# Optimization experiments

Hardware: AMD Instinct MI355X
Metric: run time of the kernel (lower is better)

Reference implementation:

```python
import jax, jax.numpy as jnp
import numpy as np

# ---- module hyperparameters (from init_kwargs) ----
B, C, T = 4, 512, 400
K = 31            # kernel_size
STRIDE = 1
WP = 3            # weight_precision -> WP-1 = 2 paired memristor arrays
# DacAdcHardwareSettings
IN_BITS = 8
OUT_PREC = 8
OUT_RANGE = 10
VMAX = 0.6
CUR_SCALE = 8020.0
DAC_SCALE = 1.0 / 2 ** (IN_BITS - 1)
DAC_MIN, DAC_MAX = -(2 ** (IN_BITS - 1)), 2 ** (IN_BITS - 1)
ADC_SCALE = 1.0 / 2 ** OUT_PREC
ADC_MIN, ADC_MAX = -(2 ** (OUT_PREC + OUT_RANGE - 1)), 2 ** (OUT_PREC + OUT_RANGE - 1)
# memristor noise model constants
KBT = 1.380649e-23 * 300.0
BW = 1e-8
E = float(np.exp(1.0))
EPS = 1e-12
INPUT_FACTOR = 1.0
OUTPUT_FACTOR = 1.0


def fake_quant(x, scale, qmin, qmax):
    # torch.fake_quantize_per_tensor_affine with zero_point=0, STE gradient inside range
    q = jnp.round(x / scale)
    qc = jnp.clip(q, qmin, qmax) * scale
    mask = (q >= qmin) & (q <= qmax)
    return jnp.where(mask, x + jax.lax.stop_gradient(qc - x), jax.lax.stop_gradient(qc))


def polyval_asc(coeffs, x):
    # coefficients in ascending degree order (as in poly_mul); Horner over static length
    res = jnp.zeros_like(x)
    for c in coeffs[::-1]:
        res = res * x + c
    return res


def setup_inputs() -> dict:
    key = jax.random.key(0)
    k1, k2, k3, k4, k5 = jax.random.split(key, 5)
    x = jax.random.normal(k1, (B, C, T), dtype=jnp.float32)
    poly_low = jax.random.normal(k2, (WP - 1, 2, 7), dtype=jnp.float32)   # [bit, pos/neg, low_degree]
    poly_high = jax.random.normal(k3, (WP - 1, 2, 6), dtype=jnp.float32)  # [bit, pos/neg, high_degree]
    r = jax.random.uniform(k4, (WP - 1, 2, C, K), dtype=jnp.float32)      # blend factor per cell
    bias = jax.random.normal(k5, (C,), dtype=jnp.float32)
    return {"x": x, "poly_low": poly_low, "poly_high": poly_high, "r": r, "bias": bias}


def reference(x, poly_low, poly_high, r, bias):
    # x: [B, C, T]
    pad = K - 1  # 'same' padding, stride 1
    pl, pr = pad // 2, pad - pad // 2
    xp = jnp.pad(x * INPUT_FACTOR, ((0, 0), (0, 0), (pl, pr)))  # zeros padding mode
    # DAC: fake quantize input, scale to hardware voltage
    v = fake_quant(xp, DAC_SCALE, DAC_MIN, DAC_MAX) * VMAX
    t_out = (T + pad - K) // STRIDE + 1
    idx = jnp.arange(t_out)[:, None] * STRIDE + jnp.arange(K)   # [T_out, K]
    w = v[:, :, idx]                                            # [B, C, T_out, K]
    w = jnp.transpose(w, (0, 2, 1, 3))                          # [B, T_out, C, K] == [...B, A=C, I=K]
    key = jax.random.key(42)
    out = jnp.zeros((B, t_out, C), dtype=x.dtype)
    for i in range(WP - 1):
        bit = WP - 2 - i  # memristors[i] carries bit (WP-2-i), per init_from_conv_quant
        pair = jnp.zeros((B, t_out, C), dtype=x.dtype)
        for s in range(2):  # 0 = pos array, 1 = neg array
            low = polyval_asc(poly_low[i, s], w)
            high = polyval_asc(poly_high[i, s], w)
            rr = r[i, s]  # [C, K], broadcasts over B, T_out (O=1 squeezed)
            raw = low * (1.0 - rr) + high * rr
            johnson = 4.0 * KBT * BW * jnp.abs(raw / (jnp.abs(w) + EPS))
            shot = 2.0 * E * BW * jnp.abs(raw)
            sigma = jnp.sqrt(johnson + shot)
            key, nk = jax.random.split(key)
            # broadcast_noise_dims=1: one noise sample shared across the batch dim
            noise = jax.random.normal(nk, raw.shape[1:], dtype=raw.dtype)
            cur = jnp.sum(raw + noise * sigma, axis=-1)  # reduce I=K -> [B, T_out, C]
            pair = pair + (cur if s == 0 else -cur)
        # ADC per paired array, weighted by the bit significance
        out = out + fake_quant(pair * CUR_SCALE, ADC_SCALE, ADC_MIN, ADC_MAX) * float(2 ** bit)
    out = out * OUTPUT_FACTOR
    out = jnp.transpose(out, (0, 2, 1)) + bias[None, :, None]   # [B, C, T_out]
    return out
```

## Files before the change

kernel.cpp:

```cpp
#include <hip/hip_runtime.h>
#include <cstdint>

#define C_DIM 512
#define T_DIM 400
#define KW 31
#define TOUT 400
#define WSROW 432
#define TPB 512
#define PPB 128
#define ROWB 48

#define WSQ_BYTES (C_DIM * WSROW * 8)
#define RT_OFF    WSQ_BYTES
#define RT_BYTES  (C_DIM * KW * 16)
#define WS_NEEDED (WSQ_BYTES + RT_BYTES)

static inline uint32_t h_rotl32(uint32_t x, int d){ return (x<<d)|(x>>(32-d)); }

static void h_threefry2x32(uint32_t k0, uint32_t k1, uint32_t x0, uint32_t x1,
                           uint32_t* o0, uint32_t* o1){
  uint32_t ks2 = k0 ^ k1 ^ 0x1BD11BDAu;
  uint32_t ks[3] = {k0, k1, ks2};
  const int rotA[4] = {13,15,26,6};
  const int rotB[4] = {17,29,16,24};
  uint32_t v0 = x0 + k0, v1 = x1 + k1;
  for (int r = 0; r < 5; ++r){
    const int* rot = (r & 1) ? rotB : rotA;
    for (int q = 0; q < 4; ++q){
      v0 += v1; v1 = h_rotl32(v1, rot[q]); v1 ^= v0;
    }
    v0 += ks[(r+1)%3];
    v1 += ks[(r+2)%3] + (uint32_t)(r+1);
  }
  *o0 = v0; *o1 = v1;
}

template<int R>
__device__ __forceinline__ void tfr4(uint32_t v0[4], uint32_t v1[4]){
  #pragma unroll
  for (int n = 0; n < 4; ++n){
    v0[n] += v1[n];
    v1[n] = (v1[n] << R) | (v1[n] >> (32 - R));
    v1[n] ^= v0[n];
  }
}

__device__ __forceinline__ void tfinj4(uint32_t v0[4], uint32_t v1[4],
                                       const uint32_t a[4], const uint32_t b[4],
                                       uint32_t cadd){
  #pragma unroll
  for (int n = 0; n < 4; ++n){ v0[n] += a[n]; v1[n] += b[n] + cadd; }
}

__device__ __forceinline__ void threefry_xor4(const uint32_t ka[4], const uint32_t kb[4],
                                              uint32_t j, uint32_t out[4]){
  uint32_t ks2[4], v0[4], v1[4];
  #pragma unroll
  for (int n = 0; n < 4; ++n){
    ks2[n] = ka[n] ^ kb[n] ^ 0x1BD11BDAu;
    v0[n] = ka[n];
    v1[n] = j + kb[n];
  }
  tfr4<13>(v0,v1); tfr4<15>(v0,v1); tfr4<26>(v0,v1); tfr4<6>(v0,v1);
  tfinj4(v0,v1,kb,ks2,1u);
  tfr4<17>(v0,v1); tfr4<29>(v0,v1); tfr4<16>(v0,v1); tfr4<24>(v0,v1);
  tfinj4(v0,v1,ks2,ka,2u);
  tfr4<13>(v0,v1); tfr4<15>(v0,v1); tfr4<26>(v0,v1); tfr4<6>(v0,v1);
  tfinj4(v0,v1,ka,kb,3u);
  tfr4<17>(v0,v1); tfr4<29>(v0,v1); tfr4<16>(v0,v1); tfr4<24>(v0,v1);
  tfinj4(v0,v1,kb,ks2,4u);
  tfr4<13>(v0,v1); tfr4<15>(v0,v1); tfr4<26>(v0,v1); tfr4<6>(v0,v1);
  tfinj4(v0,v1,ks2,ka,5u);
  #pragma unroll
  for (int n = 0; n < 4; ++n) out[n] = v0[n] ^ v1[n];
}

__device__ __forceinline__ float erfinv_fast(float x){
  float w = -0.69314718f * __builtin_amdgcn_logf((1.0f - x) * (1.0f + x));
  float p;
  if (w < 5.0f){
    w = w - 2.5f;
    p =              2.81022636e-08f;
    p = fmaf(p, w,   3.43273939e-07f);
    p = fmaf(p, w,  -3.5233877e-06f);
    p = fmaf(p, w,  -4.39150654e-06f);
    p = fmaf(p, w,   0.00021858087f);
    p = fmaf(p, w,  -0.00125372503f);
    p = fmaf(p, w,  -0.00417768164f);
    p = fmaf(p, w,   0.246640727f);
    p = fmaf(p, w,   1.50140941f);
  } else {
    w = __builtin_amdgcn_sqrtf(w) - 3.0f;
    p =             -0.000200214257f;
    p = fmaf(p, w,   0.000100950558f);
    p = fmaf(p, w,   0.00134934322f);
    p = fmaf(p, w,  -0.00367342844f);
    p = fmaf(p, w,   0.00573950773f);
    p = fmaf(p, w,  -0.0076224613f);
    p = fmaf(p, w,   0.00943887047f);
    p = fmaf(p, w,   1.00167406f);
    p = fmaf(p, w,   2.83297682f);
  }
  return p * x;
}

__global__ __launch_bounds__(256) void dac_prepass(
    const float* __restrict__ x, uint2* __restrict__ wsq)
{
  const int m = blockIdx.x * 256 + threadIdx.x;
  const int c  = m / WSROW;
  const int tp = m - c * WSROW;
  const int time = tp - 15;
  const bool inb = (time >= 0) && (time < T_DIM);
  uint32_t off[4];
  #pragma unroll
  for (int b = 0; b < 4; ++b){
    float xv = inb ? x[(b * C_DIM + c) * T_DIM + time] : 0.0f;
    float q = rintf(xv * 128.0f);
    q = fminf(fmaxf(q, -128.0f), 128.0f);
    off[b] = (uint32_t)(((int)q + 128) * ROWB);
  }
  wsq[m] = make_uint2(off[0] | (off[1] << 16), off[2] | (off[3] << 16));
}

__global__ __launch_bounds__(256) void r_prepass(
    const float* __restrict__ r, float4* __restrict__ rT)
{
  const int m = blockIdx.x * 256 + threadIdx.x;
  if (m >= C_DIM * KW) return;
  const int c = m / KW;
  const int k = m - c * KW;
  float4 v;
  v.x = r[(0 * C_DIM + c) * KW + k];
  v.y = r[(1 * C_DIM + c) * KW + k];
  v.z = r[(2 * C_DIM + c) * KW + k];
  v.w = r[(3 * C_DIM + c) * KW + k];
  rT[m] = v;
}

template<bool USE_WS>
__global__ __launch_bounds__(TPB) void memristor_main(
    const float* __restrict__ x,
    const float* __restrict__ poly_low,
    const float* __restrict__ poly_high,
    const float* __restrict__ r,
    const float* __restrict__ bias,
    const uint2* __restrict__ wsq,
    const float4* __restrict__ rT,
    float* __restrict__ out,
    uint32_t nk0a, uint32_t nk0b, uint32_t nk1a, uint32_t nk1b,
    uint32_t nk2a, uint32_t nk2b, uint32_t nk3a, uint32_t nk3b)
{
  __shared__ __align__(16) float lut[257 * 12];

  const int tid = threadIdx.x;

  if (tid < 257){
    const int qi = tid;
    const float q = (float)(qi - 128);
    const float w = (q * 0.0078125f) * 0.6f;
    #pragma unroll
    for (int is = 0; is < 4; ++is){
      const float* pl = poly_low  + is * 7;
      const float* ph = poly_high + is * 6;
      float lo = pl[6];
      lo = fmaf(lo, w, pl[5]); lo = fmaf(lo, w, pl[4]); lo = fmaf(lo, w, pl[3]);
      lo = fmaf(lo, w, pl[2]); lo = fmaf(lo, w, pl[1]); lo = fmaf(lo, w, pl[0]);
      float hi = ph[5];
      hi = fmaf(hi, w, ph[4]); hi = fmaf(hi, w, ph[3]); hi = fmaf(hi, w, ph[2]);
      hi = fmaf(hi, w, ph[1]); hi = fmaf(hi, w, ph[0]);
      lut[qi * 12 + is * 2]     = lo;
      lut[qi * 12 + is * 2 + 1] = hi - lo;
    }
    const float jf = fmaf(1.6567788e-28f,
                          __builtin_amdgcn_rcpf(fabsf(w) + 1e-12f),
                          5.4365637e-08f);
    lut[qi * 12 + 8] = __builtin_amdgcn_sqrtf(jf);
  }
  __syncthreads();

  const int l   = tid & 3;
  const int p   = tid >> 2;
  const int gid = blockIdx.x * PPB + p;
  const int c   = gid / TOUT;
  const int t   = gid - c * TOUT;
  const int k0  = l * 8;
  const int kn  = (l == 3) ? 7 : 8;

  const uint32_t ka[4] = {nk0a, nk1a, nk2a, nk3a};
  const uint32_t kb[4] = {nk0b, nk1b, nk2b, nk3b};
  const uint32_t jbase = (uint32_t)((t * C_DIM + c) * KW);

  float acc[4][4];
  #pragma unroll
  for (int b = 0; b < 4; ++b)
    #pragma unroll
    for (int is = 0; is < 4; ++is) acc[b][is] = 0.0f;

  for (int kk = 0; kk < kn; ++kk){
    const int k = k0 + kk;

    uint32_t off[4];
    float4 rv;
    if (USE_WS){
      const uint2 ld = wsq[c * WSROW + t + k];
      off[0] = ld.x & 0xFFFFu; off[1] = ld.x >> 16;
      off[2] = ld.y & 0xFFFFu; off[3] = ld.y >> 16;
      rv = rT[c * KW + k];
    } else {
      const int time = t + k - 15;
      const bool inb = (time >= 0) && (time < T_DIM);
      #pragma unroll
      for (int b = 0; b < 4; ++b){
        float xv = inb ? x[(b * C_DIM + c) * T_DIM + time] : 0.0f;
        float q = rintf(xv * 128.0f);
        q = fminf(fmaxf(q, -128.0f), 128.0f);
        off[b] = (uint32_t)(((int)q + 128) * ROWB);
      }
      rv.x = r[(0 * C_DIM + c) * KW + k];
      rv.y = r[(1 * C_DIM + c) * KW + k];
      rv.z = r[(2 * C_DIM + c) * KW + k];
      rv.w = r[(3 * C_DIM + c) * KW + k];
    }

    uint32_t bits[4];
    threefry_xor4(ka, kb, jbase + (uint32_t)k, bits);

    float noise[4];
    #pragma unroll
    for (int is = 0; is < 4; ++is){
      const float u1 = __uint_as_float((bits[is] >> 9) | 0x3f800000u) - 1.0f;
      const float uu = fmaxf(-0.99999994f, fmaf(u1, 2.0f, -0.99999994f));
      noise[is] = 1.41421356f * erfinv_fast(uu);
    }

    #pragma unroll
    for (int b = 0; b < 4; ++b){
      const float* row = (const float*)((const char*)lut + off[b]);
      const float4 A  = *(const float4*)(row);
      const float4 Bv = *(const float4*)(row + 4);
      const float sj  = row[8];
      {
        const float raw = fmaf(A.y, rv.x, A.x);
        const float s = __builtin_amdgcn_sqrtf(fabsf(raw));
        acc[b][0] = fmaf(noise[0] * sj, s, acc[b][0] + raw);
      }
      {
        const float raw = fmaf(A.w, rv.y, A.z);
        const float s = __builtin_amdgcn_sqrtf(fabsf(raw));
        acc[b][1] = fmaf(noise[1] * sj, s, acc[b][1] + raw);
      }
      {
        const float raw = fmaf(Bv.y, rv.z, Bv.x);
        const float s = __builtin_amdgcn_sqrtf(fabsf(raw));
        acc[b][2] = fmaf(noise[2] * sj, s, acc[b][2] + raw);
      }
      {
        const float raw = fmaf(Bv.w, rv.w, Bv.z);
        const float s = __builtin_amdgcn_sqrtf(fabsf(raw));
        acc[b][3] = fmaf(noise[3] * sj, s, acc[b][3] + raw);
      }
    }
  }

  float tot[4][4];
  #pragma unroll
  for (int b = 0; b < 4; ++b)
    #pragma unroll
    for (int is = 0; is < 4; ++is){
      float v = acc[b][is];
      v += __shfl_xor(v, 1);
      v += __shfl_xor(v, 2);
      tot[b][is] = v;
    }

  if (l == 0){
    const float bv = bias[c];
    #pragma unroll
    for (int b = 0; b < 4; ++b){
      float o = 0.0f;
      #pragma unroll
      for (int i = 0; i < 2; ++i){
        const float pair = tot[b][i*2+0] - tot[b][i*2+1];
        float q = rintf((pair * 8020.0f) * 256.0f);
        q = fminf(fmaxf(q, -131072.0f), 131072.0f);
        o += (q * 0.00390625f) * ((i == 0) ? 2.0f : 1.0f);
      }
      out[(b * C_DIM + c) * TOUT + t] = o + bv;
    }
  }
}

extern "C" void kernel_launch(void* const* d_in, const int* in_sizes, int n_in,
                              void* d_out, int out_size, void* d_ws, size_t ws_size,
                              hipStream_t stream) {
  const float* x         = (const float*)d_in[0];
  const float* poly_low  = (const float*)d_in[1];
  const float* poly_high = (const float*)d_in[2];
  const float* r         = (const float*)d_in[3];
  const float* bias      = (const float*)d_in[4];
  float* out             = (float*)d_out;

  uint32_t ck0 = 0u, ck1 = 42u;
  uint32_t nk[4][2];
  for (int n = 0; n < 4; ++n){
    uint32_t a0, a1, b0, b1;
    h_threefry2x32(ck0, ck1, 0u, 0u, &a0, &a1);
    h_threefry2x32(ck0, ck1, 0u, 1u, &b0, &b1);
    nk[n][0] = b0; nk[n][1] = b1;
    ck0 = a0; ck1 = a1;
  }

  const int nblocks = (C_DIM * TOUT) / PPB;

  if (ws_size >= (size_t)WS_NEEDED){
    uint2*  wsq = (uint2*)d_ws;
    float4* rT  = (float4*)((char*)d_ws + RT_OFF);
    hipLaunchKernelGGL(dac_prepass, dim3((C_DIM * WSROW) / 256), dim3(256),
                       0, stream, x, wsq);
    hipLaunchKernelGGL(r_prepass, dim3((C_DIM * KW + 255) / 256), dim3(256),
                       0, stream, r, rT);
    hipLaunchKernelGGL((memristor_main<true>), dim3(nblocks), dim3(TPB), 0, stream,
                       x, poly_low, poly_high, r, bias, wsq, rT, out,
                       nk[0][0], nk[0][1], nk[1][0], nk[1][1],
                       nk[2][0], nk[2][1], nk[3][0], nk[3][1]);
  } else {
    hipLaunchKernelGGL((memristor_main<false>), dim3(nblocks), dim3(TPB), 0, stream,
                       x, poly_low, poly_high, r, bias,
                       (const uint2*)nullptr, (const float4*)nullptr, out,
                       nk[0][0], nk[0][1], nk[1][0], nk[1][1],
                       nk[2][0], nk[2][1], nk[3][0], nk[3][1]);
  }
}
```

Measured before the change: 108.5 us.

## Vectorize noise and accumulation with packed float2 math and preload inputs

Result: slower. 327.4 us (+201.6%).

```diff
diff --git a/kernel.cpp b/kernel.cpp
--- a/kernel.cpp
+++ b/kernel.cpp
@@ -12,8 +12,10 @@
 
 #define WSQ_BYTES (C_DIM * WSROW * 8)
 #define RT_OFF    WSQ_BYTES
-#define RT_BYTES  (C_DIM * KW * 16)
+#define RT_BYTES  ((C_DIM * KW + 1) * 16)
 #define WS_NEEDED (WSQ_BYTES + RT_BYTES)
+
+typedef float f2 __attribute__((ext_vector_type(2)));
 
 static inline uint32_t h_rotl32(uint32_t x, int d){ return (x<<d)|(x>>(32-d)); }
 
@@ -75,33 +77,18 @@
   for (int n = 0; n < 4; ++n) out[n] = v0[n] ^ v1[n];
 }
 
-__device__ __forceinline__ float erfinv_fast(float x){
-  float w = -0.69314718f * __builtin_amdgcn_logf((1.0f - x) * (1.0f + x));
-  float p;
-  if (w < 5.0f){
-    w = w - 2.5f;
-    p =              2.81022636e-08f;
-    p = fmaf(p, w,   3.43273939e-07f);
-    p = fmaf(p, w,  -3.5233877e-06f);
-    p = fmaf(p, w,  -4.39150654e-06f);
-    p = fmaf(p, w,   0.00021858087f);
-    p = fmaf(p, w,  -0.00125372503f);
-    p = fmaf(p, w,  -0.00417768164f);
-    p = fmaf(p, w,   0.246640727f);
-    p = fmaf(p, w,   1.50140941f);
-  } else {
-    w = __builtin_amdgcn_sqrtf(w) - 3.0f;
-    p =             -0.000200214257f;
-    p = fmaf(p, w,   0.000100950558f);
-    p = fmaf(p, w,   0.00134934322f);
-    p = fmaf(p, w,  -0.00367342844f);
-    p = fmaf(p, w,   0.00573950773f);
-    p = fmaf(p, w,  -0.0076224613f);
-    p = fmaf(p, w,   0.00943887047f);
-    p = fmaf(p, w,   1.00167406f);
-    p = fmaf(p, w,   2.83297682f);
-  }
-  return p * x;
+__device__ __forceinline__ float erfinv_hi(float w){
+  float ws = __builtin_amdgcn_sqrtf(w) - 3.0f;
+  float p =             -0.000200214257f;
+  p = fmaf(p, ws,   0.000100950558f);
+  p = fmaf(p, ws,   0.00134934322f);
+  p = fmaf(p, ws,  -0.00367342844f);
+  p = fmaf(p, ws,   0.00573950773f);
+  p = fmaf(p, ws,  -0.0076224613f);
+  p = fmaf(p, ws,   0.00943887047f);
+  p = fmaf(p, ws,   1.00167406f);
+  p = fmaf(p, ws,   2.83297682f);
+  return p;
 }
 
 __global__ __launch_bounds__(256) void dac_prepass(
@@ -139,7 +126,7 @@
 }
 
 template<bool USE_WS>
-__global__ __launch_bounds__(TPB) void memristor_main(
+__global__ __launch_bounds__(TPB, 4) void memristor_main(
     const float* __restrict__ x,
     const float* __restrict__ poly_low,
     const float* __restrict__ poly_high,
@@ -159,6 +146,7 @@
     const int qi = tid;
     const float q = (float)(qi - 128);
     const float w = (q * 0.0078125f) * 0.6f;
+    float lov[4], div[4];
     #pragma unroll
     for (int is = 0; is < 4; ++is){
       const float* pl = poly_low  + is * 7;
@@ -169,13 +157,16 @@
       float hi = ph[5];
       hi = fmaf(hi, w, ph[4]); hi = fmaf(hi, w, ph[3]); hi = fmaf(hi, w, ph[2]);
       hi = fmaf(hi, w, ph[1]); hi = fmaf(hi, w, ph[0]);
-      lut[qi * 12 + is * 2]     = lo;
-      lut[qi * 12 + is * 2 + 1] = hi - lo;
-    }
+      lov[is] = lo; div[is] = hi - lo;
+    }
+    lut[qi*12 + 0] = lov[0]; lut[qi*12 + 1] = lov[1];
+    lut[qi*12 + 2] = div[0]; lut[qi*12 + 3] = div[1];
+    lut[qi*12 + 4] = lov[2]; lut[qi*12 + 5] = lov[3];
+    lut[qi*12 + 6] = div[2]; lut[qi*12 + 7] = div[3];
     const float jf = fmaf(1.6567788e-28f,
                           __builtin_amdgcn_rcpf(fabsf(w) + 1e-12f),
                           5.4365637e-08f);
-    lut[qi * 12 + 8] = __builtin_amdgcn_sqrtf(jf);
+    lut[qi*12 + 8] = __builtin_amdgcn_sqrtf(jf) * 1.41421356f;
   }
   __syncthreads();
 
@@ -185,31 +176,25 @@
   const int c   = gid / TOUT;
   const int t   = gid - c * TOUT;
   const int k0  = l * 8;
-  const int kn  = (l == 3) ? 7 : 8;
 
   const uint32_t ka[4] = {nk0a, nk1a, nk2a, nk3a};
   const uint32_t kb[4] = {nk0b, nk1b, nk2b, nk3b};
-  const uint32_t jbase = (uint32_t)((t * C_DIM + c) * KW);
-
-  float acc[4][4];
-  #pragma unroll
-  for (int b = 0; b < 4; ++b)
-    #pragma unroll
-    for (int is = 0; is < 4; ++is) acc[b][is] = 0.0f;
-
-  for (int kk = 0; kk < kn; ++kk){
-    const int k = k0 + kk;
-
-    uint32_t off[4];
-    float4 rv;
-    if (USE_WS){
-      const uint2 ld = wsq[c * WSROW + t + k];
-      off[0] = ld.x & 0xFFFFu; off[1] = ld.x >> 16;
-      off[2] = ld.y & 0xFFFFu; off[3] = ld.y >> 16;
-      rv = rT[c * KW + k];
-    } else {
+  const uint32_t jbase = (uint32_t)((t * C_DIM + c) * KW) + (uint32_t)k0;
+
+  uint2  wv[8];
+  float4 rv[8];
+  if (USE_WS){
+    const uint2*  wp = wsq + c * WSROW + t + k0;
+    const float4* rp = rT + c * KW + k0;
+    #pragma unroll
+    for (int kk = 0; kk < 8; ++kk){ wv[kk] = wp[kk]; rv[kk] = rp[kk]; }
+  } else {
+    #pragma unroll
+    for (int kk = 0; kk < 8; ++kk){
+      const int k = k0 + kk;
       const int time = t + k - 15;
-      const bool inb = (time >= 0) && (time < T_DIM);
+      const bool inb = (time >= 0) && (time < T_DIM) && (k < KW);
+      uint32_t off[4];
       #pragma unroll
       for (int b = 0; b < 4; ++b){
         float xv = inb ? x[(b * C_DIM + c) * T_DIM + time] : 0.0f;
@@ -217,22 +202,67 @@
         q = fminf(fmaxf(q, -128.0f), 128.0f);
         off[b] = (uint32_t)(((int)q + 128) * ROWB);
       }
-      rv.x = r[(0 * C_DIM + c) * KW + k];
-      rv.y = r[(1 * C_DIM + c) * KW + k];
-      rv.z = r[(2 * C_DIM + c) * KW + k];
-      rv.w = r[(3 * C_DIM + c) * KW + k];
-    }
+      wv[kk] = make_uint2(off[0] | (off[1] << 16), off[2] | (off[3] << 16));
+      const int kc = (k < KW) ? k : 0;
+      rv[kk].x = r[(0 * C_DIM + c) * KW + kc];
+      rv[kk].y = r[(1 * C_DIM + c) * KW + kc];
+      rv[kk].z = r[(2 * C_DIM + c) * KW + kc];
+      rv[kk].w = r[(3 * C_DIM + c) * KW + kc];
+    }
+  }
+
+  f2 acc01[4], acc23[4];
+  #pragma unroll
+  for (int b = 0; b < 4; ++b){ acc01[b] = (f2)(0.0f); acc23[b] = (f2)(0.0f); }
+
+  auto body = [&](int kk){
+    const uint2 ld = wv[kk];
+    uint32_t off[4];
+    off[0] = ld.x & 0xFFFFu; off[1] = ld.x >> 16;
+    off[2] = ld.y & 0xFFFFu; off[3] = ld.y >> 16;
+    const f2 rr01 = {rv[kk].x, rv[kk].y};
+    const f2 rr23 = {rv[kk].z, rv[kk].w};
 
     uint32_t bits[4];
-    threefry_xor4(ka, kb, jbase + (uint32_t)k, bits);
-
-    float noise[4];
-    #pragma unroll
-    for (int is = 0; is < 4; ++is){
-      const float u1 = __uint_as_float((bits[is] >> 9) | 0x3f800000u) - 1.0f;
-      const float uu = fmaxf(-0.99999994f, fmaf(u1, 2.0f, -0.99999994f));
-      noise[is] = 1.41421356f * erfinv_fast(uu);
-    }
+    threefry_xor4(ka, kb, jbase + (uint32_t)kk, bits);
+
+    const f2 u01 = { __uint_as_float((bits[0] >> 9) | 0x3f800000u),
+                     __uint_as_float((bits[1] >> 9) | 0x3f800000u) };
+    const f2 u23 = { __uint_as_float((bits[2] >> 9) | 0x3f800000u),
+                     __uint_as_float((bits[3] >> 9) | 0x3f800000u) };
+    const float LO = -0.99999994f;
+    const f2 u1_01 = u01 - 1.0f, u1_23 = u23 - 1.0f;
+    const f2 x01 = u1_01 * 2.0f + LO;
+    const f2 x23 = u1_23 * 2.0f + LO;
+    const f2 a01 = u1_01 * (-2.0f) + 1.99999994f;
+    const f2 a23 = u1_23 * (-2.0f) + 1.99999994f;
+    const f2 b01 = u1_01 * 2.0f + 5.9604645e-8f;
+    const f2 b23 = u1_23 * 2.0f + 5.9604645e-8f;
+    const f2 pr01 = a01 * b01, pr23 = a23 * b23;
+
+    const f2 w01 = { __builtin_amdgcn_logf(pr01.x) * (-0.69314718f),
+                     __builtin_amdgcn_logf(pr01.y) * (-0.69314718f) };
+    const f2 w23 = { __builtin_amdgcn_logf(pr23.x) * (-0.69314718f),
+                     __builtin_amdgcn_logf(pr23.y) * (-0.69314718f) };
+
+    const f2 t01 = w01 - 2.5f, t23 = w23 - 2.5f;
+    f2 p01 = (f2)(2.81022636e-08f), p23 = (f2)(2.81022636e-08f);
+    p01 = p01*t01 + 3.43273939e-07f;  p23 = p23*t23 + 3.43273939e-07f;
+    p01 = p01*t01 + -3.5233877e-06f;  p23 = p23*t23 + -3.5233877e-06f;
+    p01 = p01*t01 + -4.39150654e-06f; p23 = p23*t23 + -4.39150654e-06f;
+    p01 = p01*t01 + 0.00021858087f;   p23 = p23*t23 + 0.00021858087f;
+    p01 = p01*t01 + -0.00125372503f;  p23 = p23*t23 + -0.00125372503f;
+    p01 = p01*t01 + -0.00417768164f;  p23 = p23*t23 + -0.00417768164f;
+    p01 = p01*t01 + 0.246640727f;     p23 = p23*t23 + 0.246640727f;
+    p01 = p01*t01 + 1.50140941f;      p23 = p23*t23 + 1.50140941f;
+
+    if (w01.x >= 5.0f) p01.x = erfinv_hi(w01.x);
+    if (w01.y >= 5.0f) p01.y = erfinv_hi(w01.y);
+    if (w23.x >= 5.0f) p23.x = erfinv_hi(w23.x);
+    if (w23.y >= 5.0f) p23.y = erfinv_hi(w23.y);
+
+    const f2 noise01 = p01 * x01;
+    const f2 noise23 = p23 * x23;
 
     #pragma unroll
     for (int b = 0; b < 4; ++b){
@@ -240,54 +270,54 @@
       const float4 A  = *(const float4*)(row);
       const float4 Bv = *(const float4*)(row + 4);
       const float sj  = row[8];
-      {
-        const float raw = fmaf(A.y, rv.x, A.x);
-        const float s = __builtin_amdgcn_sqrtf(fabsf(raw));
-        acc[b][0] = fmaf(noise[0] * sj, s, acc[b][0] + raw);
-      }
-      {
-        const float raw = fmaf(A.w, rv.y, A.z);
-        const float s = __builtin_amdgcn_sqrtf(fabsf(raw));
-        acc[b][1] = fmaf(noise[1] * sj, s, acc[b][1] + raw);
-      }
-      {
-        const float raw = fmaf(Bv.y, rv.z, Bv.x);
-        const float s = __builtin_amdgcn_sqrtf(fabsf(raw));
-        acc[b][2] = fmaf(noise[2] * sj, s, acc[b][2] + raw);
-      }
-      {
-        const float raw = fmaf(Bv.w, rv.w, Bv.z);
-        const float s = __builtin_amdgcn_sqrtf(fabsf(raw));
-        acc[b][3] = fmaf(noise[3] * sj, s, acc[b][3] + raw);
-      }
-    }
-  }
-
-  float tot[4][4];
-  #pragma unroll
-  for (int b = 0; b < 4; ++b)
-    #pragma unroll
-    for (int is = 0; is < 4; ++is){
-      float v = acc[b][is];
-      v += __shfl_xor(v, 1);
-      v += __shfl_xor(v, 2);
-      tot[b][is] = v;
-    }
-
+      const f2 lo01 = {A.x, A.y},  d01 = {A.z, A.w};
+      const f2 lo23 = {Bv.x, Bv.y}, d23 = {Bv.z, Bv.w};
+      const f2 raw01 = d01 * rr01 + lo01;
+      const f2 raw23 = d23 * rr23 + lo23;
+      const f2 s01 = { __builtin_amdgcn_sqrtf(fabsf(raw01.x)),
+                       __builtin_amdgcn_sqrtf(fabsf(raw01.y)) };
+      const f2 s23 = { __builtin_amdgcn_sqrtf(fabsf(raw23.x)),
+                       __builtin_amdgcn_sqrtf(fabsf(raw23.y)) };
+      const f2 nsj01 = noise01 * sj;
+      const f2 nsj23 = noise23 * sj;
+      acc01[b] = nsj01 * s01 + (acc01[b] + raw01);
+      acc23[b] = nsj23 * s23 + (acc23[b] + raw23);
+    }
+  };
+
+  #pragma unroll
+  for (int kk = 0; kk < 7; ++kk) body(kk);
+  if (l != 3) body(7);
+
+  if ((p & 0) == 0) {}
+  const float bv = bias[c];
+  float o[4];
+  #pragma unroll
+  for (int b = 0; b < 4; ++b){
+    f2 t01 = acc01[b], t23 = acc23[b];
+    t01.x += __shfl_xor(t01.x, 1); t01.x += __shfl_xor(t01.x, 2);
+    t01.y += __shfl_xor(t01.y, 1); t01.y += __shfl_xor(t01.y, 2);
+    t23.x += __shfl_xor(t23.x, 1); t23.x += __shfl_xor(t23.x, 2);
+    t23.y += __shfl_xor(t23.y, 1); t23.y += __shfl_xor(t23.y, 2);
+    float oo = 0.0f;
+    {
+      const float pair = t01.x - t01.y;
+      float q = rintf((pair * 8020.0f) * 256.0f);
+      q = fminf(fmaxf(q, -131072.0f), 131072.0f);
+      oo += (q * 0.00390625f) * 2.0f;
+    }
+    {
+      const float pair = t23.x - t23.y;
+      float q = rintf((pair * 8020.0f) * 256.0f);
+      q = fminf(fmaxf(q, -131072.0f), 131072.0f);
+      oo += (q * 0.00390625f);
+    }
+    o[b] = oo + bv;
+  }
   if (l == 0){
-    const float bv = bias[c];
-    #pragma unroll
-    for (int b = 0; b < 4; ++b){
-      float o = 0.0f;
-      #pragma unroll
-      for (int i = 0; i < 2; ++i){
-        const float pair = tot[b][i*2+0] - tot[b][i*2+1];
-        float q = rintf((pair * 8020.0f) * 256.0f);
-        q = fminf(fmaxf(q, -131072.0f), 131072.0f);
-        o += (q * 0.00390625f) * ((i == 0) ? 2.0f : 1.0f);
-      }
-      out[(b * C_DIM + c) * TOUT + t] = o + bv;
-    }
+    #pragma unroll
+    for (int b = 0; b < 4; ++b)
+      out[(b * C_DIM + c) * TOUT + t] = o[b];
   }
 }
 
```
